# Optimization experiments

Hardware: AMD Instinct MI355X
Metric: run time of the kernel (lower is better)

Reference implementation:

```python
import jax, jax.numpy as jnp
import numpy as np

N = 262144       # number of samples
DIM = 64         # feature dim
NCLASSES = 128   # number of gaussian classes


def setup_inputs() -> dict:
    key = jax.random.key(0)
    k1, k2, k3, k4 = jax.random.split(key, 4)
    inputs = jax.random.normal(k1, (N, DIM), dtype=jnp.float32)
    target = jax.random.randint(k2, (N,), 0, NCLASSES)
    mean_param = jax.random.normal(k3, (NCLASSES, DIM), dtype=jnp.float32) * 0.02
    cov_param = jax.random.normal(k4, (NCLASSES, DIM, DIM), dtype=jnp.float32) * 0.02
    return {"inputs": inputs, "target": target,
            "mean_param": mean_param, "cov_param": cov_param}


def _l2_distance(sample_mean, sample_cov_sq, mean_param, cov_param):
    # Concrete stand-in for the user-supplied `distance` callable:
    # squared-L2 between the empirical class mean and the learned means,
    # plus the energy of the empirical covariance vector and learned covariances.
    return (jnp.sum((sample_mean[None, :] - mean_param) ** 2)
            + sample_cov_sq
            + jnp.sum(cov_param ** 2))


def reference(inputs, target, mean_param, cov_param):
    nclasses = mean_param.shape[0]
    n = inputs.shape[0]
    # per-class counts and means (fused segmented reduction, one pass)
    counts = jax.ops.segment_sum(jnp.ones((n,), inputs.dtype), target,
                                 num_segments=nclasses)           # [C]
    sums = jax.ops.segment_sum(inputs, target, num_segments=nclasses)  # [C, D]
    means = sums / counts[:, None]                                 # [C, D]
    # center each sample by its class mean  (torch: temp = x - mean)
    temp = inputs - means[target]                                  # [N, D]
    # torch: cov = mm(temp, temp.T).mean(0); row k equals temp_k . mean_j(temp_j)
    # so we only need the per-class sum of centered rows (analytically ~0).
    s = jax.ops.segment_sum(temp, target, num_segments=nclasses)   # [C, D]
    cov = jnp.sum(temp * s[target], axis=-1) / counts[target]      # [N] per-sample entry
    # loss in the python loop is overwritten each iter -> only last class survives
    last = nclasses - 1
    cov_sq_last = jax.ops.segment_sum(cov * cov, target, num_segments=nclasses)[last]
    loss = _l2_distance(means[last], cov_sq_last, mean_param, cov_param)
    return loss
```

## Files before the change

### kernel.cpp

```cpp
#include <hip/hip_runtime.h>


#define DIM 64
#define NCLASSES 128
#define LAST (NCLASSES - 1)
#define NBLOCKS 128
#define BLOCK 512
#define NWAVES (NBLOCKS * 8)

__global__ __launch_bounds__(BLOCK) void gem_fused(
    const float* __restrict__ inputs, const int* __restrict__ target,
    const float* __restrict__ mean_param, const float* __restrict__ cov_param,
    int n, int cov_n4, float* __restrict__ ws, float* __restrict__ out)
{
    const int tid  = threadIdx.x;
    const int lane = tid & 63;
    const int wib  = tid >> 6;
    const int b    = blockIdx.x;
    const int gwave = b * 8 + wib;

    float acc = 0.f;
    int   cnt = 0;
    for (int base = gwave * 256; base < n; base += NWAVES * 256) {
        const int4 t4 = *(const int4*)(target + base + lane * 4);
        unsigned long long m0 = __ballot(t4.x == LAST);
        unsigned long long m1 = __ballot(t4.y == LAST);
        unsigned long long m2 = __ballot(t4.z == LAST);
        unsigned long long m3 = __ballot(t4.w == LAST);
        cnt += __popcll(m0) + __popcll(m1) + __popcll(m2) + __popcll(m3);
        #pragma unroll
        for (int j = 0; j < 4; ++j) {
            unsigned long long m = (j == 0) ? m0 : (j == 1) ? m1 : (j == 2) ? m2 : m3;
            while (m) {
                int bit = __ffsll(m) - 1;
                m &= m - 1;
                acc += inputs[(size_t)(base + 4 * bit + j) * DIM + lane];
            }
        }
    }

    const float4* c4 = (const float4*)cov_param;
    float csum = 0.f;
    for (int i = b * BLOCK + tid; i < cov_n4; i += NBLOCKS * BLOCK) {
        float4 v = c4[i];
        csum += v.x * v.x + v.y * v.y + v.z * v.z + v.w * v.w;
    }
    for (int off = 32; off; off >>= 1) csum += __shfl_down(csum, off, 64);

    __shared__ float sacc[8][DIM];
    __shared__ float scov[8];
    __shared__ int   scnt[8];
    sacc[wib][lane] = acc;
    if (lane == 0) { scov[wib] = csum; scnt[wib] = cnt; }
    __syncthreads();

    if (wib == 0) {
        float s = 0.f;
        #pragma unroll
        for (int w = 0; w < 8; ++w) s += sacc[w][lane];
        atomicAdd(&ws[lane], s);
    }
    if (tid == 0) {
        int   c  = 0;   for (int w = 0; w < 8; ++w) c  += scnt[w];
        float cv = 0.f; for (int w = 0; w < 8; ++w) cv += scov[w];
        atomicAdd(&ws[DIM],     (float)c);
        atomicAdd(&ws[DIM + 1], cv);
    }

    __shared__ int amLast;
    __threadfence();
    __syncthreads();
    if (tid == 0) {
        unsigned int old = atomicAdd((unsigned int*)(ws + DIM + 2), 1u);
        amLast = (old == NBLOCKS - 1);
    }
    __syncthreads();
    if (!amLast) return;

    __shared__ float raw[DIM + 2];
    __shared__ float smean[DIM];
    if (tid < DIM + 2) raw[tid] = atomicAdd(&ws[tid], 0.f);
    __syncthreads();
    if (tid < DIM) smean[tid] = raw[tid] / raw[DIM];
    __syncthreads();

    float dacc = 0.f;
    for (int i = tid; i < NCLASSES * DIM; i += BLOCK) {
        float d = smean[i & (DIM - 1)] - mean_param[i];
        dacc += d * d;
    }
    for (int off = 32; off; off >>= 1) dacc += __shfl_down(dacc, off, 64);
    __shared__ float fr[8];
    if (lane == 0) fr[wib] = dacc;
    __syncthreads();
    if (tid == 0) {
        float t = raw[DIM + 1];
        #pragma unroll
        for (int w = 0; w < 8; ++w) t += fr[w];
        out[0] = t;
    }
}

extern "C" void kernel_launch(void* const* d_in, const int* in_sizes, int n_in,
                              void* d_out, int out_size, void* d_ws, size_t ws_size,
                              hipStream_t stream) {
    const float* inputs     = (const float*)d_in[0];
    const int*   target     = (const int*)d_in[1];
    const float* mean_param = (const float*)d_in[2];
    const float* cov_param  = (const float*)d_in[3];
    float* out = (float*)d_out;
    float* ws  = (float*)d_ws;

    const int n     = in_sizes[0] / DIM;
    const int cov_n = in_sizes[3];

    hipMemsetAsync(d_ws, 0, (DIM + 3) * sizeof(float), stream);
    gem_fused<<<NBLOCKS, BLOCK, 0, stream>>>(inputs, target, mean_param, cov_param,
                                             n, cov_n / 4, ws, out);
}
```

Measured before the change: 116.4 us.

## Replace atomics and last-block detection with per-block partials and a finalize kernel

Each block now writes its partial sums to its own workspace slot instead of using float atomics, and a second single-block kernel reduces them. This removes the memset, the atomic contention and the threadfence/last-block counter. The mean-distance term is expanded algebraically so block 0 precomputes column sums and the sum of squares of mean_param, and the finalize step uses only these. The cost is an extra kernel launch, plus extra work on block 0, and the expanded form can lose a little floating-point accuracy.

```diff
diff --git a/kernel.cpp b/kernel.cpp
--- a/kernel.cpp
+++ b/kernel.cpp
@@ -7,11 +7,13 @@
 #define NBLOCKS 128
 #define BLOCK 512
 #define NWAVES (NBLOCKS * 8)
+#define SLOT 68
+#define COLBASE (NBLOCKS * SLOT)
 
-__global__ __launch_bounds__(BLOCK) void gem_fused(
+__global__ __launch_bounds__(BLOCK) void gem_part(
     const float* __restrict__ inputs, const int* __restrict__ target,
     const float* __restrict__ mean_param, const float* __restrict__ cov_param,
-    int n, int cov_n4, float* __restrict__ ws, float* __restrict__ out)
+    int n, int cov_n4, float* __restrict__ ws)
 {
     const int tid  = threadIdx.x;
     const int lane = tid & 63;
@@ -47,57 +49,84 @@
     }
     for (int off = 32; off; off >>= 1) csum += __shfl_down(csum, off, 64);
 
+    float pcol = 0.f, psq = 0.f;
+    if (b == 0) {
+        #pragma unroll
+        for (int k = 0; k < (NCLASSES * DIM) / BLOCK; ++k) {
+            float v = mean_param[tid + k * BLOCK];
+            pcol += v;
+            psq  += v * v;
+        }
+    }
+    for (int off = 32; off; off >>= 1) psq += __shfl_down(psq, off, 64);
+
     __shared__ float sacc[8][DIM];
-    __shared__ float scov[8];
+    __shared__ float scol[8][DIM];
+    __shared__ float scov[8], spsq[8];
     __shared__ int   scnt[8];
     sacc[wib][lane] = acc;
-    if (lane == 0) { scov[wib] = csum; scnt[wib] = cnt; }
+    scol[wib][lane] = pcol;
+    if (lane == 0) { scov[wib] = csum; scnt[wib] = cnt; spsq[wib] = psq; }
     __syncthreads();
 
     if (wib == 0) {
         float s = 0.f;
         #pragma unroll
         for (int w = 0; w < 8; ++w) s += sacc[w][lane];
-        atomicAdd(&ws[lane], s);
+        ws[b * SLOT + lane] = s;
+        if (b == 0) {
+            float cs = 0.f;
+            #pragma unroll
+            for (int w = 0; w < 8; ++w) cs += scol[w][lane];
+            ws[COLBASE + lane] = cs;
+        }
     }
     if (tid == 0) {
-        int   c  = 0;   for (int w = 0; w < 8; ++w) c  += scnt[w];
-        float cv = 0.f; for (int w = 0; w < 8; ++w) cv += scov[w];
-        atomicAdd(&ws[DIM],     (float)c);
-        atomicAdd(&ws[DIM + 1], cv);
+        int   c  = 0;   float cv = 0.f, q = 0.f;
+        #pragma unroll
+        for (int w = 0; w < 8; ++w) { c += scnt[w]; cv += scov[w]; q += spsq[w]; }
+        ws[b * SLOT + DIM]     = (float)c;
+        ws[b * SLOT + DIM + 1] = cv;
+        if (b == 0) ws[COLBASE + DIM] = q;
+    }
+}
+
+__global__ __launch_bounds__(BLOCK) void gem_final(
+    const float* __restrict__ ws, float* __restrict__ out)
+{
+    const int tid  = threadIdx.x;
+    const int lane = tid & 63;
+    const int g    = tid >> 6;
+
+    float s = 0.f;
+    #pragma unroll
+    for (int j = 0; j < NBLOCKS / 8; ++j)
+        s += ws[(g + 8 * j) * SLOT + lane];
+
+    float c = 0.f, cv = 0.f;
+    if (tid < NBLOCKS) { c = ws[tid * SLOT + DIM]; cv = ws[tid * SLOT + DIM + 1]; }
+    for (int off = 32; off; off >>= 1) {
+        c  += __shfl_down(c,  off, 64);
+        cv += __shfl_down(cv, off, 64);
     }
 
-    __shared__ int amLast;
-    __threadfence();
-    __syncthreads();
-    if (tid == 0) {
-        unsigned int old = atomicAdd((unsigned int*)(ws + DIM + 2), 1u);
-        amLast = (old == NBLOCKS - 1);
-    }
-    __syncthreads();
-    if (!amLast) return;
-
-    __shared__ float raw[DIM + 2];
-    __shared__ float smean[DIM];
-    if (tid < DIM + 2) raw[tid] = atomicAdd(&ws[tid], 0.f);
-    __syncthreads();
-    if (tid < DIM) smean[tid] = raw[tid] / raw[DIM];
+    __shared__ float red[8][DIM];
+    __shared__ float scc[2][2];
+    red[g][lane] = s;
+    if (tid < NBLOCKS && lane == 0) { scc[g][0] = c; scc[g][1] = cv; }
     __syncthreads();
 
-    float dacc = 0.f;
-    for (int i = tid; i < NCLASSES * DIM; i += BLOCK) {
-        float d = smean[i & (DIM - 1)] - mean_param[i];
-        dacc += d * d;
-    }
-    for (int off = 32; off; off >>= 1) dacc += __shfl_down(dacc, off, 64);
-    __shared__ float fr[8];
-    if (lane == 0) fr[wib] = dacc;
-    __syncthreads();
-    if (tid == 0) {
-        float t = raw[DIM + 1];
+    if (tid < DIM) {
+        float tot = 0.f;
         #pragma unroll
-        for (int w = 0; w < 8; ++w) t += fr[w];
-        out[0] = t;
+        for (int w = 0; w < 8; ++w) tot += red[w][tid];
+        const float count = scc[0][0] + scc[1][0];
+        const float covs  = scc[0][1] + scc[1][1];
+        const float mean  = tot / count;
+        const float col   = ws[COLBASE + tid];
+        float d = (float)NCLASSES * mean * mean - 2.f * mean * col;
+        for (int off = 32; off; off >>= 1) d += __shfl_down(d, off, 64);
+        if (tid == 0) out[0] = d + covs + ws[COLBASE + DIM];
     }
 }
 
@@ -114,7 +143,7 @@
     const int n     = in_sizes[0] / DIM;
     const int cov_n = in_sizes[3];
 
-    hipMemsetAsync(d_ws, 0, (DIM + 3) * sizeof(float), stream);
-    gem_fused<<<NBLOCKS, BLOCK, 0, stream>>>(inputs, target, mean_param, cov_param,
-                                             n, cov_n / 4, ws, out);
+    gem_part<<<NBLOCKS, BLOCK, 0, stream>>>(inputs, target, mean_param, cov_param,
+                                            n, cov_n / 4, ws);
+    gem_final<<<1, BLOCK, 0, stream>>>(ws, out);
 }
```

After: 95.57 us. -17.9%, faster.
